# Performance work log

Hardware: AMD Instinct MI355X
Metric: run time of the kernel (lower is better)

## Reference

```python
import jax, jax.numpy as jnp
import numpy as np

# (multiplicity, irrep_dim) for irreps_in == irreps_out: 128x0e + 64x1o + 32x2e
IRREPS = [(128, 1), (64, 3), (32, 5)]
NUM_INDICES = 64
N_ELEMENTS = 8192
SCALE = 1.0  # module's `scale` arg; total coeff = scale / sqrt(num_indices) / sqrt(mul_in)
W_DIM = sum(m * m for m, _ in IRREPS)  # 21504


def setup_inputs() -> dict:
    key = jax.random.key(0)
    ks = jax.random.split(key, 5)
    x0 = jax.random.normal(ks[0], (N_ELEMENTS, 128, 1), jnp.float32)
    x1 = jax.random.normal(ks[1], (N_ELEMENTS, 64, 3), jnp.float32)
    x2 = jax.random.normal(ks[2], (N_ELEMENTS, 32, 5), jnp.float32)
    w = jax.random.normal(ks[3], (NUM_INDICES, W_DIM), jnp.float32)
    # Random contiguous segment sizes that sum exactly to N_ELEMENTS:
    bnd = jnp.sort(jax.random.randint(ks[4], (NUM_INDICES - 1,), 0, N_ELEMENTS + 1)).astype(jnp.int32)
    counts = jnp.diff(jnp.concatenate([jnp.zeros((1,), jnp.int32), bnd,
                                       jnp.full((1,), N_ELEMENTS, jnp.int32)]))
    return {"x0": x0, "x1": x1, "x2": x2, "w": w, "num_index_counts": counts}


def reference(x0, x1, x2, w, num_index_counts):
    """Indexed (segmented) equivariant linear: rows are grouped contiguously by
    num_index_counts; segment g uses weight row w[g]. Per matched irrep the
    weight block is a (mul_in, mul_out) mixing matrix applied identically to
    each of the ir.dim components (Schur's lemma), with fan-in normalization
    1/sqrt(mul_in) (cue.descriptors.linear) times scale/sqrt(num_indices)."""
    n = x0.shape[0]
    # segment id per row (rows are already grouped contiguously, as in Repeats())
    sid = jnp.repeat(jnp.arange(NUM_INDICES), num_index_counts, total_repeat_length=n)
    xs = (x0, x1, x2)
    ys = []
    off = 0
    for xk, (mul, ir_dim) in zip(xs, IRREPS):
        blk = w[:, off:off + mul * mul].reshape(NUM_INDICES, mul, mul)  # (E, m_in, m_out)
        coeff = float(SCALE / np.sqrt(NUM_INDICES) / np.sqrt(mul))
        wk = blk[sid]  # (n, m_in, m_out) per-row weight gather
        # y[n, o, i] = coeff * sum_m x[n, m, i] * w[g(n), m, o]
        ys.append(coeff * jnp.einsum('nmi,nmo->noi', xk, wk))
        off += mul * mul
    return tuple(ys)
```

## Files before the change

### kernel.cpp

```cpp
#include <hip/hip_runtime.h>

#define NSEG 64
#define NROW 8192
#define TILE 16
#define WROW 21504

#define P0 132
#define P1 196
#define P2 164

__global__ __launch_bounds__(256) void iil_kernel(
    const float* __restrict__ x0, const float* __restrict__ x1, const float* __restrict__ x2,
    const float* __restrict__ w, const int* __restrict__ counts,
    float* __restrict__ y0, float* __restrict__ y1, float* __restrict__ y2)
{
    __shared__ float sx0[TILE * P0];
    __shared__ float sx1[TILE * P1];
    __shared__ float sx2[TILE * P2];
    __shared__ int sstart[NSEG + 1];
    __shared__ int ssid[TILE];

    const int t = threadIdx.x;
    const int row0 = blockIdx.x * TILE;

    if (t < NSEG) {
        int v = counts[t];
        #pragma unroll
        for (int d = 1; d < NSEG; d <<= 1) {
            int u = __shfl_up(v, d, 64);
            if (t >= d) v += u;
        }
        sstart[t + 1] = v;
        if (t == 0) sstart[0] = 0;
    }
    if (t < TILE) {
        int r = row0 + t;
        int lo = 0, hi = NSEG;
        while (hi - lo > 1) {
            int mid = (lo + hi) >> 1;
            if (sstart[mid] <= r) lo = mid; else hi = mid;
        }
        ssid[t] = lo;
    }

    {
        const float4* g0 = (const float4*)x0 + (size_t)row0 * 32;
        float4* s0 = (float4*)sx0;
        #pragma unroll
        for (int i = 0; i < 2; ++i) {
            int idx = t + i * 256;
            int r = idx >> 5, c = idx & 31;
            s0[r * (P0 / 4) + c] = g0[idx];
        }
        const float4* g1 = (const float4*)x1 + (size_t)row0 * 48;
        float4* s1 = (float4*)sx1;
        #pragma unroll
        for (int i = 0; i < 3; ++i) {
            int idx = t + i * 256;
            int r = idx / 48, c = idx - r * 48;
            s1[r * (P1 / 4) + c] = g1[idx];
        }
        const float4* g2 = (const float4*)x2 + (size_t)row0 * 40;
        float4* s2 = (float4*)sx2;
        #pragma unroll
        for (int i = 0; i < 3; ++i) {
            int idx = t + i * 256;
            if (idx < 640) {
                int r = idx / 40, c = idx - r * 40;
                s2[r * (P2 / 4) + c] = g2[idx];
            }
        }
    }
    __syncthreads();

    {
        const int og = t & 31;
        const int rg = t >> 5;
        const int r0 = rg * 2, r1 = r0 + 1;
        const float* wp0 = w + (size_t)ssid[r0] * WROW + og * 4;
        const float* wp1 = w + (size_t)ssid[r1] * WROW + og * 4;
        const float* xr0 = sx0 + r0 * P0;
        const float* xr1 = sx0 + r1 * P0;
        float4 a0 = make_float4(0.f, 0.f, 0.f, 0.f);
        float4 a1 = make_float4(0.f, 0.f, 0.f, 0.f);
        #pragma unroll 4
        for (int k = 0; k < 128; ++k) {
            float xa = xr0[k];
            float xb = xr1[k];
            float4 w0v = *(const float4*)(wp0 + (size_t)k * 128);
            float4 w1v = *(const float4*)(wp1 + (size_t)k * 128);
            a0.x = fmaf(xa, w0v.x, a0.x);
            a0.y = fmaf(xa, w0v.y, a0.y);
            a0.z = fmaf(xa, w0v.z, a0.z);
            a0.w = fmaf(xa, w0v.w, a0.w);
            a1.x = fmaf(xb, w1v.x, a1.x);
            a1.y = fmaf(xb, w1v.y, a1.y);
            a1.z = fmaf(xb, w1v.z, a1.z);
            a1.w = fmaf(xb, w1v.w, a1.w);
        }
        const float c0 = 0.011048543456039806f;
        float4 o0 = make_float4(a0.x * c0, a0.y * c0, a0.z * c0, a0.w * c0);
        float4 o1 = make_float4(a1.x * c0, a1.y * c0, a1.z * c0, a1.w * c0);
        *(float4*)(y0 + (size_t)(row0 + r0) * 128 + og * 4) = o0;
        *(float4*)(y0 + (size_t)(row0 + r1) * 128 + og * 4) = o1;
    }

    {
        const int og = t & 15;
        const int r  = t >> 4;
        const float* wp = w + (size_t)ssid[r] * WROW + 16384 + og * 4;
        const float* xr = sx1 + r * P1;
        float acc[12];
        #pragma unroll
        for (int i = 0; i < 12; ++i) acc[i] = 0.f;
        #pragma unroll 4
        for (int k = 0; k < 64; ++k) {
            float xi0 = xr[k * 3 + 0];
            float xi1 = xr[k * 3 + 1];
            float xi2 = xr[k * 3 + 2];
            float4 wv = *(const float4*)(wp + (size_t)k * 64);
            acc[0]  = fmaf(wv.x, xi0, acc[0]);
            acc[1]  = fmaf(wv.x, xi1, acc[1]);
            acc[2]  = fmaf(wv.x, xi2, acc[2]);
            acc[3]  = fmaf(wv.y, xi0, acc[3]);
            acc[4]  = fmaf(wv.y, xi1, acc[4]);
            acc[5]  = fmaf(wv.y, xi2, acc[5]);
            acc[6]  = fmaf(wv.z, xi0, acc[6]);
            acc[7]  = fmaf(wv.z, xi1, acc[7]);
            acc[8]  = fmaf(wv.z, xi2, acc[8]);
            acc[9]  = fmaf(wv.w, xi0, acc[9]);
            acc[10] = fmaf(wv.w, xi1, acc[10]);
            acc[11] = fmaf(wv.w, xi2, acc[11]);
        }
        const float c1 = 0.015625f;
        float* yb = y1 + (size_t)(row0 + r) * 192 + og * 12;
        float4 v0 = make_float4(acc[0] * c1, acc[1] * c1, acc[2] * c1, acc[3] * c1);
        float4 v1 = make_float4(acc[4] * c1, acc[5] * c1, acc[6] * c1, acc[7] * c1);
        float4 v2 = make_float4(acc[8] * c1, acc[9] * c1, acc[10] * c1, acc[11] * c1);
        *(float4*)(yb + 0) = v0;
        *(float4*)(yb + 4) = v1;
        *(float4*)(yb + 8) = v2;
    }

    {
        const int og = t & 15;
        const int r  = t >> 4;
        const float* wp = w + (size_t)ssid[r] * WROW + 20480 + og * 2;
        const float* xr = sx2 + r * P2;
        float acc[10];
        #pragma unroll
        for (int i = 0; i < 10; ++i) acc[i] = 0.f;
        #pragma unroll 4
        for (int k = 0; k < 32; ++k) {
            float xv[5];
            #pragma unroll
            for (int i = 0; i < 5; ++i) xv[i] = xr[k * 5 + i];
            float2 wv = *(const float2*)(wp + (size_t)k * 32);
            #pragma unroll
            for (int i = 0; i < 5; ++i) {
                acc[i]     = fmaf(wv.x, xv[i], acc[i]);
                acc[5 + i] = fmaf(wv.y, xv[i], acc[5 + i]);
            }
        }
        const float c2 = 0.022097086912079608f;
        float* yb = y2 + (size_t)(row0 + r) * 160 + og * 10;
        #pragma unroll
        for (int i = 0; i < 5; ++i) {
            float2 v = make_float2(acc[2 * i] * c2, acc[2 * i + 1] * c2);
            *(float2*)(yb + 2 * i) = v;
        }
    }
}

extern "C" void kernel_launch(void* const* d_in, const int* in_sizes, int n_in,
                              void* d_out, int out_size, void* d_ws, size_t ws_size,
                              hipStream_t stream) {
    const float* x0 = (const float*)d_in[0];
    const float* x1 = (const float*)d_in[1];
    const float* x2 = (const float*)d_in[2];
    const float* w  = (const float*)d_in[3];
    const int* counts = (const int*)d_in[4];

    float* y0 = (float*)d_out;
    float* y1 = y0 + (size_t)NROW * 128;
    float* y2 = y1 + (size_t)NROW * 192;

    hipLaunchKernelGGL(iil_kernel, dim3(NROW / TILE), dim3(256), 0, stream,
                       x0, x1, x2, w, counts, y0, y1, y2);
}
```

Baseline: 100.2 us.

## Assign tiles per segment so each block uses one weight row, stage weights in LDS

Blocks are now mapped to segment-aligned tiles through a prefix sum over per-segment tile counts, so every block serves rows of a single segment and partial tiles are masked. This removes per-row weight gathers in which two rows in a tile could read different weight rows. The l=0 path now computes a 4-row by 2-output register tile from a transposed x tile, the l=1 weight block is cached in shared memory, and x reads are vectorised. The cost is up to 64 extra partially filled blocks, early-exit blocks, and larger shared memory use, which may lower occupancy.

```diff
diff --git a/kernel.cpp b/kernel.cpp
--- a/kernel.cpp
+++ b/kernel.cpp
@@ -4,170 +4,202 @@
 #define NROW 8192
 #define TILE 16
 #define WROW 21504
-
-#define P0 132
-#define P1 196
-#define P2 164
+#define NBLK 576
+
+#define PT0 20
+#define P1  196
+#define P2  164
 
 __global__ __launch_bounds__(256) void iil_kernel(
     const float* __restrict__ x0, const float* __restrict__ x1, const float* __restrict__ x2,
     const float* __restrict__ w, const int* __restrict__ counts,
     float* __restrict__ y0, float* __restrict__ y1, float* __restrict__ y2)
 {
-    __shared__ float sx0[TILE * P0];
+    __shared__ float xT0[128 * PT0];
     __shared__ float sx1[TILE * P1];
     __shared__ float sx2[TILE * P2];
+    __shared__ float w1s[64 * 64];
     __shared__ int sstart[NSEG + 1];
-    __shared__ int ssid[TILE];
+    __shared__ int tstart[NSEG + 1];
 
     const int t = threadIdx.x;
-    const int row0 = blockIdx.x * TILE;
 
     if (t < NSEG) {
-        int v = counts[t];
+        int c = counts[t];
+        int v = c;
         #pragma unroll
         for (int d = 1; d < NSEG; d <<= 1) {
             int u = __shfl_up(v, d, 64);
             if (t >= d) v += u;
         }
         sstart[t + 1] = v;
-        if (t == 0) sstart[0] = 0;
-    }
-    if (t < TILE) {
-        int r = row0 + t;
-        int lo = 0, hi = NSEG;
-        while (hi - lo > 1) {
-            int mid = (lo + hi) >> 1;
-            if (sstart[mid] <= r) lo = mid; else hi = mid;
-        }
-        ssid[t] = lo;
-    }
-
-    {
-        const float4* g0 = (const float4*)x0 + (size_t)row0 * 32;
-        float4* s0 = (float4*)sx0;
+        int tcv = (c + TILE - 1) >> 4;
+        #pragma unroll
+        for (int d = 1; d < NSEG; d <<= 1) {
+            int u = __shfl_up(tcv, d, 64);
+            if (t >= d) tcv += u;
+        }
+        tstart[t + 1] = tcv;
+        if (t == 0) { sstart[0] = 0; tstart[0] = 0; }
+    }
+    __syncthreads();
+
+    const int b = blockIdx.x;
+    if (b >= tstart[NSEG]) return;
+
+    int lo = 0, hi = NSEG;
+    while (hi - lo > 1) {
+        int mid = (lo + hi) >> 1;
+        if (tstart[mid] <= b) lo = mid; else hi = mid;
+    }
+    const int g = lo;
+    const int s = sstart[g] + (b - tstart[g]) * TILE;
+    const int nr = min(TILE, sstart[g + 1] - s);
+    const float* __restrict__ wseg = w + (size_t)g * WROW;
+
+    {
+        const float4 z4 = make_float4(0.f, 0.f, 0.f, 0.f);
+        const float4* g0 = (const float4*)x0 + (size_t)s * 32;
         #pragma unroll
         for (int i = 0; i < 2; ++i) {
             int idx = t + i * 256;
-            int r = idx >> 5, c = idx & 31;
-            s0[r * (P0 / 4) + c] = g0[idx];
-        }
-        const float4* g1 = (const float4*)x1 + (size_t)row0 * 48;
-        float4* s1 = (float4*)sx1;
+            int r = idx >> 5, c4 = idx & 31;
+            float4 v = (r < nr) ? g0[idx] : z4;
+            xT0[(c4 * 4 + 0) * PT0 + r] = v.x;
+            xT0[(c4 * 4 + 1) * PT0 + r] = v.y;
+            xT0[(c4 * 4 + 2) * PT0 + r] = v.z;
+            xT0[(c4 * 4 + 3) * PT0 + r] = v.w;
+        }
+        const float4* g1 = (const float4*)x1 + (size_t)s * 48;
         #pragma unroll
         for (int i = 0; i < 3; ++i) {
             int idx = t + i * 256;
             int r = idx / 48, c = idx - r * 48;
-            s1[r * (P1 / 4) + c] = g1[idx];
-        }
-        const float4* g2 = (const float4*)x2 + (size_t)row0 * 40;
-        float4* s2 = (float4*)sx2;
+            float4 v = (r < nr) ? g1[idx] : z4;
+            *(float4*)(sx1 + r * P1 + c * 4) = v;
+        }
+        const float4* g2 = (const float4*)x2 + (size_t)s * 40;
         #pragma unroll
         for (int i = 0; i < 3; ++i) {
             int idx = t + i * 256;
             if (idx < 640) {
                 int r = idx / 40, c = idx - r * 40;
-                s2[r * (P2 / 4) + c] = g2[idx];
-            }
+                float4 v = (r < nr) ? g2[idx] : z4;
+                *(float4*)(sx2 + r * P2 + c * 4) = v;
+            }
+        }
+        const float4* gw1 = (const float4*)(wseg + 16384);
+        #pragma unroll
+        for (int i = 0; i < 4; ++i) {
+            int idx = t + i * 256;
+            *(float4*)(w1s + idx * 4) = gw1[idx];
         }
     }
     __syncthreads();
 
     {
-        const int og = t & 31;
-        const int rg = t >> 5;
-        const int r0 = rg * 2, r1 = r0 + 1;
-        const float* wp0 = w + (size_t)ssid[r0] * WROW + og * 4;
-        const float* wp1 = w + (size_t)ssid[r1] * WROW + og * 4;
-        const float* xr0 = sx0 + r0 * P0;
-        const float* xr1 = sx0 + r1 * P0;
-        float4 a0 = make_float4(0.f, 0.f, 0.f, 0.f);
-        float4 a1 = make_float4(0.f, 0.f, 0.f, 0.f);
+        const int og = t & 63;
+        const int rg = t >> 6;
+        const float* wp = wseg + og * 2;
+        const float* xb = xT0 + rg * 4;
+        float acc[8];
+        #pragma unroll
+        for (int i = 0; i < 8; ++i) acc[i] = 0.f;
         #pragma unroll 4
         for (int k = 0; k < 128; ++k) {
-            float xa = xr0[k];
-            float xb = xr1[k];
-            float4 w0v = *(const float4*)(wp0 + (size_t)k * 128);
-            float4 w1v = *(const float4*)(wp1 + (size_t)k * 128);
-            a0.x = fmaf(xa, w0v.x, a0.x);
-            a0.y = fmaf(xa, w0v.y, a0.y);
-            a0.z = fmaf(xa, w0v.z, a0.z);
-            a0.w = fmaf(xa, w0v.w, a0.w);
-            a1.x = fmaf(xb, w1v.x, a1.x);
-            a1.y = fmaf(xb, w1v.y, a1.y);
-            a1.z = fmaf(xb, w1v.z, a1.z);
-            a1.w = fmaf(xb, w1v.w, a1.w);
+            float4 xv = *(const float4*)(xb + k * PT0);
+            float2 wv = *(const float2*)(wp + (size_t)k * 128);
+            acc[0] = fmaf(xv.x, wv.x, acc[0]);
+            acc[1] = fmaf(xv.x, wv.y, acc[1]);
+            acc[2] = fmaf(xv.y, wv.x, acc[2]);
+            acc[3] = fmaf(xv.y, wv.y, acc[3]);
+            acc[4] = fmaf(xv.z, wv.x, acc[4]);
+            acc[5] = fmaf(xv.z, wv.y, acc[5]);
+            acc[6] = fmaf(xv.w, wv.x, acc[6]);
+            acc[7] = fmaf(xv.w, wv.y, acc[7]);
         }
         const float c0 = 0.011048543456039806f;
-        float4 o0 = make_float4(a0.x * c0, a0.y * c0, a0.z * c0, a0.w * c0);
-        float4 o1 = make_float4(a1.x * c0, a1.y * c0, a1.z * c0, a1.w * c0);
-        *(float4*)(y0 + (size_t)(row0 + r0) * 128 + og * 4) = o0;
-        *(float4*)(y0 + (size_t)(row0 + r1) * 128 + og * 4) = o1;
+        #pragma unroll
+        for (int jr = 0; jr < 4; ++jr) {
+            int r = rg * 4 + jr;
+            if (r < nr) {
+                float2 v = make_float2(acc[jr * 2] * c0, acc[jr * 2 + 1] * c0);
+                *(float2*)(y0 + (size_t)(s + r) * 128 + og * 2) = v;
+            }
+        }
     }
 
     {
         const int og = t & 15;
-        const int r  = t >> 4;
-        const float* wp = w + (size_t)ssid[r] * WROW + 16384 + og * 4;
-        const float* xr = sx1 + r * P1;
+        const int r = t >> 4;
+        const float* xrow = sx1 + r * P1;
         float acc[12];
         #pragma unroll
         for (int i = 0; i < 12; ++i) acc[i] = 0.f;
-        #pragma unroll 4
-        for (int k = 0; k < 64; ++k) {
-            float xi0 = xr[k * 3 + 0];
-            float xi1 = xr[k * 3 + 1];
-            float xi2 = xr[k * 3 + 2];
-            float4 wv = *(const float4*)(wp + (size_t)k * 64);
-            acc[0]  = fmaf(wv.x, xi0, acc[0]);
-            acc[1]  = fmaf(wv.x, xi1, acc[1]);
-            acc[2]  = fmaf(wv.x, xi2, acc[2]);
-            acc[3]  = fmaf(wv.y, xi0, acc[3]);
-            acc[4]  = fmaf(wv.y, xi1, acc[4]);
-            acc[5]  = fmaf(wv.y, xi2, acc[5]);
-            acc[6]  = fmaf(wv.z, xi0, acc[6]);
-            acc[7]  = fmaf(wv.z, xi1, acc[7]);
-            acc[8]  = fmaf(wv.z, xi2, acc[8]);
-            acc[9]  = fmaf(wv.w, xi0, acc[9]);
-            acc[10] = fmaf(wv.w, xi1, acc[10]);
-            acc[11] = fmaf(wv.w, xi2, acc[11]);
+        #pragma unroll 2
+        for (int kq = 0; kq < 16; ++kq) {
+            float4 xq0 = *(const float4*)(xrow + 12 * kq + 0);
+            float4 xq1 = *(const float4*)(xrow + 12 * kq + 4);
+            float4 xq2 = *(const float4*)(xrow + 12 * kq + 8);
+            float xf[12] = {xq0.x, xq0.y, xq0.z, xq0.w,
+                            xq1.x, xq1.y, xq1.z, xq1.w,
+                            xq2.x, xq2.y, xq2.z, xq2.w};
+            #pragma unroll
+            for (int kk = 0; kk < 4; ++kk) {
+                int k = 4 * kq + kk;
+                float4 wv = *(const float4*)(w1s + k * 64 + og * 4);
+                #pragma unroll
+                for (int oo = 0; oo < 4; ++oo) {
+                    float wvo = (oo == 0) ? wv.x : (oo == 1) ? wv.y : (oo == 2) ? wv.z : wv.w;
+                    acc[oo * 3 + 0] = fmaf(wvo, xf[kk * 3 + 0], acc[oo * 3 + 0]);
+                    acc[oo * 3 + 1] = fmaf(wvo, xf[kk * 3 + 1], acc[oo * 3 + 1]);
+                    acc[oo * 3 + 2] = fmaf(wvo, xf[kk * 3 + 2], acc[oo * 3 + 2]);
+                }
+            }
         }
         const float c1 = 0.015625f;
-        float* yb = y1 + (size_t)(row0 + r) * 192 + og * 12;
-        float4 v0 = make_float4(acc[0] * c1, acc[1] * c1, acc[2] * c1, acc[3] * c1);
-        float4 v1 = make_float4(acc[4] * c1, acc[5] * c1, acc[6] * c1, acc[7] * c1);
-        float4 v2 = make_float4(acc[8] * c1, acc[9] * c1, acc[10] * c1, acc[11] * c1);
-        *(float4*)(yb + 0) = v0;
-        *(float4*)(yb + 4) = v1;
-        *(float4*)(yb + 8) = v2;
+        if (r < nr) {
+            float* yb = y1 + (size_t)(s + r) * 192 + og * 12;
+            *(float4*)(yb + 0) = make_float4(acc[0] * c1, acc[1] * c1, acc[2] * c1, acc[3] * c1);
+            *(float4*)(yb + 4) = make_float4(acc[4] * c1, acc[5] * c1, acc[6] * c1, acc[7] * c1);
+            *(float4*)(yb + 8) = make_float4(acc[8] * c1, acc[9] * c1, acc[10] * c1, acc[11] * c1);
+        }
     }
 
     {
         const int og = t & 15;
-        const int r  = t >> 4;
-        const float* wp = w + (size_t)ssid[r] * WROW + 20480 + og * 2;
-        const float* xr = sx2 + r * P2;
+        const int r = t >> 4;
+        const float* xrow = sx2 + r * P2;
+        const float* wp = wseg + 20480 + og * 2;
         float acc[10];
         #pragma unroll
         for (int i = 0; i < 10; ++i) acc[i] = 0.f;
-        #pragma unroll 4
-        for (int k = 0; k < 32; ++k) {
-            float xv[5];
-            #pragma unroll
-            for (int i = 0; i < 5; ++i) xv[i] = xr[k * 5 + i];
-            float2 wv = *(const float2*)(wp + (size_t)k * 32);
+        #pragma unroll
+        for (int kq = 0; kq < 8; ++kq) {
+            float xf[20];
+            #pragma unroll
+            for (int j = 0; j < 5; ++j) {
+                float4 v = *(const float4*)(xrow + 20 * kq + 4 * j);
+                xf[4 * j + 0] = v.x; xf[4 * j + 1] = v.y; xf[4 * j + 2] = v.z; xf[4 * j + 3] = v.w;
+            }
+            #pragma unroll
+            for (int kk = 0; kk < 4; ++kk) {
+                int k = 4 * kq + kk;
+                float2 wv = *(const float2*)(wp + (size_t)k * 32);
+                #pragma unroll
+                for (int i = 0; i < 5; ++i) {
+                    acc[i]     = fmaf(wv.x, xf[5 * kk + i], acc[i]);
+                    acc[5 + i] = fmaf(wv.y, xf[5 * kk + i], acc[5 + i]);
+                }
+            }
+        }
+        const float c2 = 0.022097086912079608f;
+        if (r < nr) {
+            float* yb = y2 + (size_t)(s + r) * 160 + og * 10;
             #pragma unroll
             for (int i = 0; i < 5; ++i) {
-                acc[i]     = fmaf(wv.x, xv[i], acc[i]);
-                acc[5 + i] = fmaf(wv.y, xv[i], acc[5 + i]);
-            }
-        }
-        const float c2 = 0.022097086912079608f;
-        float* yb = y2 + (size_t)(row0 + r) * 160 + og * 10;
-        #pragma unroll
-        for (int i = 0; i < 5; ++i) {
-            float2 v = make_float2(acc[2 * i] * c2, acc[2 * i + 1] * c2);
-            *(float2*)(yb + 2 * i) = v;
+                *(float2*)(yb + 2 * i) = make_float2(acc[2 * i] * c2, acc[2 * i + 1] * c2);
+            }
         }
     }
 }
@@ -185,6 +217,6 @@
     float* y1 = y0 + (size_t)NROW * 128;
     float* y2 = y1 + (size_t)NROW * 192;
 
-    hipLaunchKernelGGL(iil_kernel, dim3(NROW / TILE), dim3(256), 0, stream,
+    hipLaunchKernelGGL(iil_kernel, dim3(NBLK), dim3(256), 0, stream,
                        x0, x1, x2, w, counts, y0, y1, y2);
 }
```

New measurement: 111.6 us. +11.4%, slower.
